# Kernel optimization log

Measured on AMD Instinct MI355X. Metric: run time of the kernel, lower is better.

## Reference

```python
import jax, jax.numpy as jnp
import numpy as np

TEMPERATURE = 8.0  # sqrt(head_dim=64)
NEG_INF = -1e9


def setup_inputs() -> dict:
    key = jax.random.key(0)
    kq, kk, kv, km = jax.random.split(key, 4)
    B, H, S, D = 4, 16, 2048, 64
    q = jax.random.normal(kq, (B, H, S, D), dtype=jnp.float32)
    k = jax.random.normal(kk, (B, H, S, D), dtype=jnp.float32)
    v = jax.random.normal(kv, (B, H, S, D), dtype=jnp.float32)
    mask = jax.random.randint(km, (B, 1, S, S), 0, 2).astype(jnp.int32)
    return {"q": q, "k": k, "v": v, "mask": mask}


def reference(q, k, v, mask):
    # attn = (q / T) @ k^T  -> [B,H,S,S]
    attn = jnp.einsum('bhqd,bhkd->bhqk', q / TEMPERATURE, k)
    # masked_fill(mask == 0, -1e9)
    attn = jnp.where(mask == 0, NEG_INF, attn)
    # softmax over keys (dropout omitted: eval mode / deterministic baseline)
    attn = jax.nn.softmax(attn, axis=-1)
    out = jnp.einsum('bhqk,bhkd->bhqd', attn, v)
    return (out, attn)
```

## Files before the change

### kernel.cpp

```cpp
#include <hip/hip_runtime.h>
#include <stdint.h>

#define S_LEN 2048
#define DHEAD 64
#define BATCH 4
#define HEADS 16
#define QBLK 32
#define KBLK 64
#define NT 32
#define NBLK 4096
#define NEG_BIG (-1e9f)

typedef _Float16 half4v __attribute__((ext_vector_type(4)));
typedef _Float16 half8v __attribute__((ext_vector_type(8)));
typedef float floatx4 __attribute__((ext_vector_type(4)));

#define QH_OFF 0u
#define KH_OFF 16777216u
#define VT_OFF 33554432u
#define BM_OFF 50331648u

#define WAITV(N) asm volatile("s_waitcnt vmcnt(" #N ")" ::: "memory")
#define WAITL()  asm volatile("s_waitcnt lgkmcnt(0)" ::: "memory")
#define FENCE()  asm volatile("" ::: "memory")
#define BAR()    __builtin_amdgcn_s_barrier()

__device__ __forceinline__ void glds16(const void* g, void* l) {
    __builtin_amdgcn_global_load_lds(
        (const __attribute__((address_space(1))) uint32_t*)g,
        (__attribute__((address_space(3))) uint32_t*)(uint32_t)(uintptr_t)l,
        16, 0, 0);
}

__global__ __launch_bounds__(256) void prep_qk(const float* __restrict__ q, const float* __restrict__ k,
                                               _Float16* __restrict__ qh, _Float16* __restrict__ kh) {
    int i = blockIdx.x * 256 + threadIdx.x;
    const float* src; _Float16* dst; float s;
    if (i < 1048576) { src = q + (size_t)i * 8; dst = qh + (size_t)i * 8; s = 0.125f; }
    else { int j = i - 1048576; src = k + (size_t)j * 8; dst = kh + (size_t)j * 8; s = 1.0f; }
    floatx4 a = *(const floatx4*)src;
    floatx4 b = *(const floatx4*)(src + 4);
    half8v h;
    h[0]=(_Float16)(a[0]*s); h[1]=(_Float16)(a[1]*s); h[2]=(_Float16)(a[2]*s); h[3]=(_Float16)(a[3]*s);
    h[4]=(_Float16)(b[0]*s); h[5]=(_Float16)(b[1]*s); h[6]=(_Float16)(b[2]*s); h[7]=(_Float16)(b[3]*s);
    *(half8v*)dst = h;
}

__global__ __launch_bounds__(256) void prep_vt(const float* __restrict__ v, _Float16* __restrict__ vt) {
    __shared__ _Float16 lt[64][72];
    int bh = blockIdx.x >> 5;
    int s0 = (blockIdx.x & 31) * 64;
    int t  = threadIdx.x;
    {
        int row = t >> 2, dq = t & 3;
        const float* vb = v + ((size_t)bh * S_LEN + s0 + row) * DHEAD + dq * 16;
        #pragma unroll
        for (int q = 0; q < 4; ++q) {
            floatx4 val = *(const floatx4*)(vb + q * 4);
            #pragma unroll
            for (int j = 0; j < 4; ++j) lt[dq * 16 + q * 4 + j][row] = (_Float16)val[j];
        }
    }
    __syncthreads();
    {
        int d = t >> 2, kq = t & 3;
        half8v h0 = *(const half8v*)&lt[d][kq * 16];
        half8v h1 = *(const half8v*)&lt[d][kq * 16 + 8];
        _Float16* dst = vt + (size_t)bh * DHEAD * S_LEN + (size_t)d * S_LEN + s0 + kq * 16;
        *(half8v*)dst = h0;
        *(half8v*)(dst + 8) = h1;
    }
}

__global__ __launch_bounds__(256) void prep_bm(const int* __restrict__ mask, unsigned long long* __restrict__ bm) {
    int lane = threadIdx.x & 63, w = threadIdx.x >> 6;
    size_t row = (size_t)blockIdx.x * 4 + w;
    const int* mrow = mask + row * S_LEN;
    unsigned long long* brow = bm + row * 32;
    #pragma unroll 4
    for (int t = 0; t < 32; ++t) {
        unsigned long long bits = __ballot(mrow[t * 64 + lane] != 0);
        if (lane == 0) brow[t] = bits;
    }
}

__global__ __launch_bounds__(512, 8)
void attn_main(const _Float16* __restrict__ qh, const _Float16* __restrict__ kh,
               const _Float16* __restrict__ vt, const uint32_t* __restrict__ bm,
               float* __restrict__ outg, float* __restrict__ attng)
{
    __shared__ __attribute__((aligned(16))) char smem[37376];
    char* kbuf = smem;
    char* vbuf = smem + 16384;
    char* pb   = smem + 32768;
    float* zbf = (float*)(smem + 36864);

    const int tid  = threadIdx.x;
    const int lane = tid & 63;
    const int w    = tid >> 6;
    const int c    = lane & 15;
    const int g    = lane >> 4;
    const int kg   = w & 3;
    const int rh   = w >> 2;

    const int raw = blockIdx.x;
    const int lb  = (raw & 7) * (NBLK / 8) + (raw >> 3);
    const int bh  = lb >> 6;
    const int q0  = (lb & 63) * QBLK;
    const int bb  = bh >> 4;

    const _Float16* qp = qh + (size_t)bh * S_LEN * DHEAD;
    const char* kpc = (const char*)(kh + (size_t)bh * S_LEN * DHEAD);
    const char* vpc = (const char*)(vt + (size_t)bh * DHEAD * S_LEN);
    float* outp  = outg  + (size_t)bh * S_LEN * DHEAD;
    float* attnp = attng + (size_t)bh * S_LEN * S_LEN;

    const int srow = tid >> 3;
    const int sq   = (lane & 7) ^ (srow & 7);
    const char* ksrc = kpc + srow * 128 + sq * 16;
    const char* vsrc = vpc + srow * (S_LEN * 2) + sq * 16;
    char* kdst = kbuf + w * 1024;
    char* vdst = vbuf + w * 1024;

    half8v qf0, qf1;
    {
        const _Float16* qb = qp + (q0 + rh * 16 + c) * DHEAD + g * 8;
        qf0 = *(const half8v*)qb;
        qf1 = *(const half8v*)(qb + 32);
    }
    const int koff0 = (kg * 16 + c) * 128 + ((g ^ (c & 7)) << 4);
    const int koff1 = (kg * 16 + c) * 128 + (((4 + g) ^ (c & 7)) << 4);
    const int prow  = rh * 16 + c;
    const int poff0 = prow * 128 + ((g ^ (c & 7)) << 4);
    const int poff1 = prow * 128 + (((4 + g) ^ (c & 7)) << 4);
    const int koff0p = c * 128 + ((g ^ (c & 7)) << 4);
    const int koff1p = c * 128 + (((4 + g) ^ (c & 7)) << 4);

    const int bmbit = (kg & 1) * 16 + c;
    const uint32_t* bmb = bm + ((size_t)bb * S_LEN + q0 + rh * 16 + g * 4) * 64 + (kg >> 1);

    int pwo0, pwo1, pwo2, pwo3;
    {
        int keyl = kg * 16 + c;
        int q8 = keyl >> 3, b2 = (keyl & 7) << 1;
        int r0 = rh * 16 + g * 4;
        pwo0 = (((r0 + 0) * 8 + (q8 ^ ((r0 + 0) & 7))) << 4) + b2;
        pwo1 = (((r0 + 1) * 8 + (q8 ^ ((r0 + 1) & 7))) << 4) + b2;
        pwo2 = (((r0 + 2) * 8 + (q8 ^ ((r0 + 2) & 7))) << 4) + b2;
        pwo3 = (((r0 + 3) * 8 + (q8 ^ ((r0 + 3) & 7))) << 4) + b2;
    }
    const int ar = tid >> 4, aq = tid & 15;
    const int proff = ar * 128 + (((aq >> 1) ^ (ar & 7)) << 4) + ((aq & 1) << 3);
    float* abase = attnp + (size_t)(q0 + ar) * S_LEN + aq * 4;

    float z0 = 0.f, z1 = 0.f, z2 = 0.f, z3 = 0.f;
    char* myb = smem + w * 4096;
    const char* kps = kpc + kg * 2048 + (lane >> 3) * 128
                    + (((lane & 7) ^ ((lane >> 3) & 7)) << 4);
    glds16(kps, myb);
    glds16(kps + 1024, myb + 1024);
    FENCE();
    uint32_t bc0 = bmb[0], bc1 = bmb[64], bc2 = bmb[128], bc3 = bmb[192];
    FENCE();
    glds16(kps + 8192, myb + 2048);
    glds16(kps + 9216, myb + 3072);
    FENCE();
    uint32_t bn0 = 0, bn1 = 0, bn2 = 0, bn3 = 0;
    #pragma unroll 1
    for (int t = 0; t < NT; ++t) {
        FENCE();
        if (t == NT - 1) { WAITV(0); } else { WAITV(2); }
        char* kbB = myb + ((t & 1) << 11);
        half8v kf0 = *(const half8v*)(kbB + koff0p);
        half8v kf1 = *(const half8v*)(kbB + koff1p);
        WAITL(); FENCE();
        if (t + 1 < NT) {
            int i2 = (t + 1) * 2;
            bn0 = bmb[i2]; bn1 = bmb[64 + i2]; bn2 = bmb[128 + i2]; bn3 = bmb[192 + i2];
            FENCE();
        }
        if (t + 2 < NT) {
            const char* s = kps + (t + 2) * 8192;
            glds16(s, kbB);
            glds16(s + 1024, kbB + 1024);
            FENCE();
        }
        floatx4 acc = {0.f, 0.f, 0.f, 0.f};
        acc = __builtin_amdgcn_mfma_f32_16x16x32_f16(qf0, kf0, acc, 0, 0, 0);
        acc = __builtin_amdgcn_mfma_f32_16x16x32_f16(qf1, kf1, acc, 0, 0, 0);
        z0 += __expf(((bc0 >> bmbit) & 1u) ? acc[0] : NEG_BIG);
        z1 += __expf(((bc1 >> bmbit) & 1u) ? acc[1] : NEG_BIG);
        z2 += __expf(((bc2 >> bmbit) & 1u) ? acc[2] : NEG_BIG);
        z3 += __expf(((bc3 >> bmbit) & 1u) ? acc[3] : NEG_BIG);
        bc0 = bn0; bc1 = bn1; bc2 = bn2; bc3 = bn3;
    }
    #pragma unroll
    for (int off = 1; off <= 8; off <<= 1) {
        z0 += __shfl_xor(z0, off); z1 += __shfl_xor(z1, off);
        z2 += __shfl_xor(z2, off); z3 += __shfl_xor(z3, off);
    }
    if (c == 0) {
        int r0 = rh * 16 + g * 4;
        zbf[kg * 32 + r0] = z0; zbf[kg * 32 + r0 + 1] = z1;
        zbf[kg * 32 + r0 + 2] = z2; zbf[kg * 32 + r0 + 3] = z3;
    }
    WAITL(); BAR(); FENCE();
    float r0_, r1_, r2_, r3_;
    {
        int r0 = rh * 16 + g * 4;
        r0_ = 1.f / (zbf[r0] + zbf[32 + r0] + zbf[64 + r0] + zbf[96 + r0]);
        r1_ = 1.f / (zbf[r0+1] + zbf[32 + r0+1] + zbf[64 + r0+1] + zbf[96 + r0+1]);
        r2_ = 1.f / (zbf[r0+2] + zbf[32 + r0+2] + zbf[64 + r0+2] + zbf[96 + r0+2]);
        r3_ = 1.f / (zbf[r0+3] + zbf[32 + r0+3] + zbf[64 + r0+3] + zbf[96 + r0+3]);
    }
    BAR(); FENCE();

    floatx4 o = {0.f, 0.f, 0.f, 0.f};
    glds16(ksrc, kdst);
    glds16(vsrc, vdst);
    FENCE();
    bc0 = bmb[0]; bc1 = bmb[64]; bc2 = bmb[128]; bc3 = bmb[192];
    #pragma unroll 1
    for (int t = 0; t < NT; ++t) {
        BAR(); FENCE();
        if (t + 1 < NT) {
            glds16(ksrc + (t + 1) * 8192, kdst + (((t + 1) & 1) << 13));
            glds16(vsrc + (t + 1) * 128,  vdst + (((t + 1) & 1) << 13));
            int i2 = (t + 1) * 2;
            bn0 = bmb[i2]; bn1 = bmb[64 + i2]; bn2 = bmb[128 + i2]; bn3 = bmb[192 + i2];
            if (t == 0) { WAITV(6); } else { WAITV(7); }
        } else { WAITV(1); }
        BAR(); FENCE();
        const char* kbB = kbuf + ((t & 1) << 13);
        const char* vbB = vbuf + ((t & 1) << 13);
        half8v b0 = *(const half8v*)(kbB + koff0);
        half8v b1 = *(const half8v*)(kbB + koff1);
        floatx4 acc = {0.f, 0.f, 0.f, 0.f};
        acc = __builtin_amdgcn_mfma_f32_16x16x32_f16(qf0, b0, acc, 0, 0, 0);
        acc = __builtin_amdgcn_mfma_f32_16x16x32_f16(qf1, b1, acc, 0, 0, 0);
        float p0 = __expf(((bc0 >> bmbit) & 1u) ? acc[0] : NEG_BIG) * r0_;
        float p1 = __expf(((bc1 >> bmbit) & 1u) ? acc[1] : NEG_BIG) * r1_;
        float p2 = __expf(((bc2 >> bmbit) & 1u) ? acc[2] : NEG_BIG) * r2_;
        float p3 = __expf(((bc3 >> bmbit) & 1u) ? acc[3] : NEG_BIG) * r3_;
        bc0 = bn0; bc1 = bn1; bc2 = bn2; bc3 = bn3;
        *(_Float16*)(pb + pwo0) = (_Float16)p0;
        *(_Float16*)(pb + pwo1) = (_Float16)p1;
        *(_Float16*)(pb + pwo2) = (_Float16)p2;
        *(_Float16*)(pb + pwo3) = (_Float16)p3;
        WAITL(); BAR(); FENCE();
        {
            half4v pv4 = *(const half4v*)(pb + proff);
            floatx4 st = {(float)pv4[0], (float)pv4[1], (float)pv4[2], (float)pv4[3]};
            __builtin_nontemporal_store(st, (floatx4*)(abase + t * KBLK));
        }
        half8v a0 = *(const half8v*)(pb + poff0);
        half8v a1 = *(const half8v*)(pb + poff1);
        half8v v0 = *(const half8v*)(vbB + koff0);
        half8v v1 = *(const half8v*)(vbB + koff1);
        o = __builtin_amdgcn_mfma_f32_16x16x32_f16(a0, v0, o, 0, 0, 0);
        o = __builtin_amdgcn_mfma_f32_16x16x32_f16(a1, v1, o, 0, 0, 0);
    }
    {
        float* ob = outp + (size_t)(q0 + rh * 16 + g * 4) * DHEAD + kg * 16 + c;
        ob[0] = o[0]; ob[DHEAD] = o[1]; ob[2 * DHEAD] = o[2]; ob[3 * DHEAD] = o[3];
    }
}

extern "C" void kernel_launch(void* const* d_in, const int* in_sizes, int n_in,
                              void* d_out, int out_size, void* d_ws, size_t ws_size,
                              hipStream_t stream) {
    const float* q    = (const float*)d_in[0];
    const float* k    = (const float*)d_in[1];
    const float* v    = (const float*)d_in[2];
    const int*   mask = (const int*)d_in[3];
    float* out  = (float*)d_out;
    float* attn = out + (size_t)BATCH * HEADS * S_LEN * DHEAD;

    char* ws = (char*)d_ws;
    _Float16* qhw = (_Float16*)(ws + QH_OFF);
    _Float16* khw = (_Float16*)(ws + KH_OFF);
    _Float16* vtw = (_Float16*)(ws + VT_OFF);
    unsigned long long* bmw = (unsigned long long*)(ws + BM_OFF);

    prep_qk<<<dim3(8192), dim3(256), 0, stream>>>(q, k, qhw, khw);
    prep_vt<<<dim3(2048), dim3(256), 0, stream>>>(v, vtw);
    prep_bm<<<dim3(2048), dim3(256), 0, stream>>>(mask, bmw);
    attn_main<<<dim3(NBLK), dim3(512), 0, stream>>>(qhw, khw, vtw, (const uint32_t*)bmw, out, attn);
}
```

Baseline: 380.9 us.

## Merge prep kernels into one launch and drop a barrier per key tile

Folds the three preprocessing kernels into a single launch that dispatches on block index, removing two kernel launches and their inter-kernel gaps. In the main loop, the wait for the current tile's async LDS loads now happens before the top barrier, which removes the second barrier per iteration. This reduces synchronisation overhead, but the prefetch of the next tile is now issued after the wait, so less load latency is overlapped and the vmcnt accounting has to stay correct.

```diff
diff --git a/kernel.cpp b/kernel.cpp
--- a/kernel.cpp
+++ b/kernel.cpp
@@ -32,55 +32,58 @@
         16, 0, 0);
 }
 
-__global__ __launch_bounds__(256) void prep_qk(const float* __restrict__ q, const float* __restrict__ k,
-                                               _Float16* __restrict__ qh, _Float16* __restrict__ kh) {
-    int i = blockIdx.x * 256 + threadIdx.x;
-    const float* src; _Float16* dst; float s;
-    if (i < 1048576) { src = q + (size_t)i * 8; dst = qh + (size_t)i * 8; s = 0.125f; }
-    else { int j = i - 1048576; src = k + (size_t)j * 8; dst = kh + (size_t)j * 8; s = 1.0f; }
-    floatx4 a = *(const floatx4*)src;
-    floatx4 b = *(const floatx4*)(src + 4);
-    half8v h;
-    h[0]=(_Float16)(a[0]*s); h[1]=(_Float16)(a[1]*s); h[2]=(_Float16)(a[2]*s); h[3]=(_Float16)(a[3]*s);
-    h[4]=(_Float16)(b[0]*s); h[5]=(_Float16)(b[1]*s); h[6]=(_Float16)(b[2]*s); h[7]=(_Float16)(b[3]*s);
-    *(half8v*)dst = h;
-}
-
-__global__ __launch_bounds__(256) void prep_vt(const float* __restrict__ v, _Float16* __restrict__ vt) {
+__global__ __launch_bounds__(256) void prep_all(const float* __restrict__ q, const float* __restrict__ k,
+                                                const float* __restrict__ v, const int* __restrict__ mask,
+                                                _Float16* __restrict__ qh, _Float16* __restrict__ kh,
+                                                _Float16* __restrict__ vt, unsigned long long* __restrict__ bm) {
     __shared__ _Float16 lt[64][72];
-    int bh = blockIdx.x >> 5;
-    int s0 = (blockIdx.x & 31) * 64;
-    int t  = threadIdx.x;
-    {
-        int row = t >> 2, dq = t & 3;
-        const float* vb = v + ((size_t)bh * S_LEN + s0 + row) * DHEAD + dq * 16;
-        #pragma unroll
-        for (int q = 0; q < 4; ++q) {
-            floatx4 val = *(const floatx4*)(vb + q * 4);
+    const int blk = blockIdx.x;
+    if (blk < 8192) {
+        int i = blk * 256 + threadIdx.x;
+        const float* src; _Float16* dst; float s;
+        if (i < 1048576) { src = q + (size_t)i * 8; dst = qh + (size_t)i * 8; s = 0.125f; }
+        else { int j = i - 1048576; src = k + (size_t)j * 8; dst = kh + (size_t)j * 8; s = 1.0f; }
+        floatx4 a = *(const floatx4*)src;
+        floatx4 b = *(const floatx4*)(src + 4);
+        half8v h;
+        h[0]=(_Float16)(a[0]*s); h[1]=(_Float16)(a[1]*s); h[2]=(_Float16)(a[2]*s); h[3]=(_Float16)(a[3]*s);
+        h[4]=(_Float16)(b[0]*s); h[5]=(_Float16)(b[1]*s); h[6]=(_Float16)(b[2]*s); h[7]=(_Float16)(b[3]*s);
+        *(half8v*)dst = h;
+    } else if (blk < 10240) {
+        int bb2 = blk - 8192;
+        int bh = bb2 >> 5;
+        int s0 = (bb2 & 31) * 64;
+        int t  = threadIdx.x;
+        {
+            int row = t >> 2, dq = t & 3;
+            const float* vb = v + ((size_t)bh * S_LEN + s0 + row) * DHEAD + dq * 16;
             #pragma unroll
-            for (int j = 0; j < 4; ++j) lt[dq * 16 + q * 4 + j][row] = (_Float16)val[j];
-        }
-    }
-    __syncthreads();
-    {
-        int d = t >> 2, kq = t & 3;
-        half8v h0 = *(const half8v*)&lt[d][kq * 16];
-        half8v h1 = *(const half8v*)&lt[d][kq * 16 + 8];
-        _Float16* dst = vt + (size_t)bh * DHEAD * S_LEN + (size_t)d * S_LEN + s0 + kq * 16;
-        *(half8v*)dst = h0;
-        *(half8v*)(dst + 8) = h1;
-    }
-}
-
-__global__ __launch_bounds__(256) void prep_bm(const int* __restrict__ mask, unsigned long long* __restrict__ bm) {
-    int lane = threadIdx.x & 63, w = threadIdx.x >> 6;
-    size_t row = (size_t)blockIdx.x * 4 + w;
-    const int* mrow = mask + row * S_LEN;
-    unsigned long long* brow = bm + row * 32;
-    #pragma unroll 4
-    for (int t = 0; t < 32; ++t) {
-        unsigned long long bits = __ballot(mrow[t * 64 + lane] != 0);
-        if (lane == 0) brow[t] = bits;
+            for (int qq = 0; qq < 4; ++qq) {
+                floatx4 val = *(const floatx4*)(vb + qq * 4);
+                #pragma unroll
+                for (int j = 0; j < 4; ++j) lt[dq * 16 + qq * 4 + j][row] = (_Float16)val[j];
+            }
+        }
+        __syncthreads();
+        {
+            int d = t >> 2, kq = t & 3;
+            half8v h0 = *(const half8v*)&lt[d][kq * 16];
+            half8v h1 = *(const half8v*)&lt[d][kq * 16 + 8];
+            _Float16* dst = vt + (size_t)bh * DHEAD * S_LEN + (size_t)d * S_LEN + s0 + kq * 16;
+            *(half8v*)dst = h0;
+            *(half8v*)(dst + 8) = h1;
+        }
+    } else {
+        int bb2 = blk - 10240;
+        int lane = threadIdx.x & 63, w = threadIdx.x >> 6;
+        size_t row = (size_t)bb2 * 4 + w;
+        const int* mrow = mask + row * S_LEN;
+        unsigned long long* brow = bm + row * 32;
+        #pragma unroll 4
+        for (int t = 0; t < 32; ++t) {
+            unsigned long long bits = __ballot(mrow[t * 64 + lane] != 0);
+            if (lane == 0) brow[t] = bits;
+        }
     }
 }
 
@@ -220,17 +223,20 @@
     glds16(vsrc, vdst);
     FENCE();
     bc0 = bmb[0]; bc1 = bmb[64]; bc2 = bmb[128]; bc3 = bmb[192];
+    FENCE();
     #pragma unroll 1
     for (int t = 0; t < NT; ++t) {
+        FENCE();
+        if (t == 0) { WAITV(4); } else { WAITV(5); }
         BAR(); FENCE();
         if (t + 1 < NT) {
             glds16(ksrc + (t + 1) * 8192, kdst + (((t + 1) & 1) << 13));
             glds16(vsrc + (t + 1) * 128,  vdst + (((t + 1) & 1) << 13));
+            FENCE();
             int i2 = (t + 1) * 2;
             bn0 = bmb[i2]; bn1 = bmb[64 + i2]; bn2 = bmb[128 + i2]; bn3 = bmb[192 + i2];
-            if (t == 0) { WAITV(6); } else { WAITV(7); }
-        } else { WAITV(1); }
-        BAR(); FENCE();
+            FENCE();
+        }
         const char* kbB = kbuf + ((t & 1) << 13);
         const char* vbB = vbuf + ((t & 1) << 13);
         half8v b0 = *(const half8v*)(kbB + koff0);
@@ -282,8 +288,6 @@
     _Float16* vtw = (_Float16*)(ws + VT_OFF);
     unsigned long long* bmw = (unsigned long long*)(ws + BM_OFF);
 
-    prep_qk<<<dim3(8192), dim3(256), 0, stream>>>(q, k, qhw, khw);
-    prep_vt<<<dim3(2048), dim3(256), 0, stream>>>(v, vtw);
-    prep_bm<<<dim3(2048), dim3(256), 0, stream>>>(mask, bmw);
+    prep_all<<<dim3(12288), dim3(256), 0, stream>>>(q, k, v, mask, qhw, khw, vtw, bmw);
     attn_main<<<dim3(NBLK), dim3(512), 0, stream>>>(qhw, khw, vtw, (const uint32_t*)bmw, out, attn);
 }
```

Result: slower. 446.0 us (+17.1%).
